# Performance work log

Measured on AMD Instinct MI355X. Metric: run time of the kernel, lower is better.

The kernel has to match this reference:

```python
import jax, jax.numpy as jnp
import numpy as np
import math

B, L, D, A, VD, H = 8, 2048, 1024, 1024, 1024, 1024
EPS = 1e-5

def gelu(x):
    return 0.5 * x * (1.0 + jax.lax.erf(x / math.sqrt(2.0)))

def setup_inputs() -> dict:
    key = jax.random.key(0)
    ks = jax.random.split(key, 12)
    s = 0.02
    return {
        "Q": jax.random.normal(ks[0], (B, L, D), jnp.float32),
        "K": jax.random.normal(ks[1], (B, L, D), jnp.float32),
        "V": jax.random.normal(ks[2], (B, L, D), jnp.float32),
        "attn_mask": jax.random.randint(ks[3], (B, L, L), 0, 2, jnp.int32),
        "Wq": jax.random.normal(ks[4], (D, A), jnp.float32) * s,
        "bq": jnp.zeros((A,), jnp.float32),
        "Wk": jax.random.normal(ks[5], (D, A), jnp.float32) * s,
        "bk": jnp.zeros((A,), jnp.float32),
        "Wv": jax.random.normal(ks[6], (D, VD), jnp.float32) * s,
        "bv": jnp.zeros((VD,), jnp.float32),
        "Wo": jax.random.normal(ks[7], (VD, H), jnp.float32) * s,
        "bo": jnp.zeros((H,), jnp.float32),
        "gamma": jnp.ones((H,), jnp.float32),
        "beta": jnp.zeros((H,), jnp.float32),
    }

def reference(Q, K, V, attn_mask, Wq, bq, Wk, bk, Wv, bv, Wo, bo, gamma, beta):
    q = Q @ Wq + bq                      # [B,L,A]
    k = K @ Wk + bk                      # [B,L,A]
    scores = jnp.einsum('bqa,bka->bqk', q, k) / math.sqrt(A)
    scores = scores + attn_mask.astype(jnp.float32) * (-1e9)
    scores = jnp.swapaxes(scores, -1, -2)  # [B,Lk,Lq]; softmax over QUERY axis
    attn = jax.nn.softmax(scores, axis=-1)
    wv = V @ Wv + bv                     # [B,L,VD]
    context = jnp.einsum('bkq,bqv->bkv', attn, wv)  # [B,L,VD]
    context = gelu(context @ Wo + bo)    # [B,L,H]
    mu = jnp.mean(context, axis=-1, keepdims=True)
    var = jnp.var(context, axis=-1, keepdims=True)
    context = (context - mu) / jnp.sqrt(var + EPS) * gamma + beta
    return context, attn
```

## Files before the change

### kernel.cpp

```cpp
#include <hip/hip_runtime.h>
#include <math.h>

typedef __bf16 bf16;
typedef __bf16 bf16x8 __attribute__((ext_vector_type(8)));
typedef __bf16 bf16x4 __attribute__((ext_vector_type(4)));
typedef float f32x4 __attribute__((ext_vector_type(4)));

__device__ inline void gload16(const void* g, void* l) {
  typedef __attribute__((address_space(1))) const unsigned int guint;
  typedef __attribute__((address_space(3))) unsigned int luint;
  __builtin_amdgcn_global_load_lds((guint*)g, (luint*)l, 16, 0, 0);
}

template<int BIAS_MODE, bool MASK, bool GELU, bool OUT_BF16>
__global__ __launch_bounds__(512, 2)
void bgemm8_k(const bf16* __restrict__ A, const bf16* __restrict__ B,
              const float* __restrict__ bias, const signed char* __restrict__ mT,
              void* __restrict__ Cout, int N, int ldc, int K,
              long sAb, long sBb, long sCb, long sMb, float scale)
{
  __shared__ bf16 As[4 * 8192];
  __shared__ bf16 Bs[4 * 8192];

  const int t    = threadIdx.x;
  const int zb   = blockIdx.z;
  const int gx   = gridDim.x;
  const int nwg  = gx * gridDim.y;
  const int orig = blockIdx.y * gx + blockIdx.x;
  const int swz  = (orig & 7) * (nwg >> 3) + (orig >> 3);
  const int m0   = (swz / gx) * 256;
  const int n0   = (swz % gx) * 256;

  const int wave = t >> 6;
  const int lane = t & 63;
  const int wm = wave >> 2;
  const int wn = wave & 3;
  const int fr = lane & 15;
  const int fg = lane >> 4;

  const bf16* Abase = A + (size_t)zb * sAb + (size_t)m0 * K;
  const bf16* Bbase = B + (size_t)zb * sBb + (size_t)n0 * K;
  size_t gOff[2];
  int    ldsOff[2];
#pragma unroll
  for (int j = 0; j < 2; ++j) {
    const int L   = j * 8192 + t * 16;
    const int row = L >> 6;
    const int gp  = (L >> 4) & 3;
    const int g   = gp ^ ((row >> 1) & 3);
    gOff[j]   = (size_t)row * K + (size_t)g * 8;
    ldsOff[j] = j * 4096 + wave * 512;
  }
  const int HMAX = (K >> 5) * 2;

  auto stage = [&](int H) {
    if (H >= HMAX) return;
    const int s    = H >> 1;
    const int slot = s & 3;
    const size_t kof = (size_t)s * 32;
    if ((H & 1) == 0) {
      gload16(Abase + kof + gOff[0], As + slot * 8192 + ldsOff[0]);
      gload16(Abase + kof + gOff[1], As + slot * 8192 + ldsOff[1]);
    } else {
      gload16(Bbase + kof + gOff[0], Bs + slot * 8192 + ldsOff[0]);
      gload16(Bbase + kof + gOff[1], Bs + slot * 8192 + ldsOff[1]);
    }
  };

  const int xsw  = (fg ^ ((fr >> 1) & 3)) * 8;
  const int aoff = (wm * 128 + fr) * 32 + xsw;
  const int boff = (wn * 64 + fr) * 32 + xsw;

  f32x4 acc[8][4] = {};
  const int T = K >> 6;

  stage(0); stage(1); stage(2); stage(3); stage(4);
  asm volatile("s_waitcnt vmcnt(6)" ::: "memory");
  __builtin_amdgcn_s_barrier();

  for (int tt = 0; tt < T; ++tt) {
#pragma unroll
    for (int p = 0; p < 4; ++p) {
      const int kk   = p & 1;
      const int oh   = p >> 1;
      const int slot = (2 * tt + kk) & 3;
      bf16x8 af[4], bfv[4];
#pragma unroll
      for (int i = 0; i < 4; ++i)
        af[i]  = *(const bf16x8*)(As + slot * 8192 + aoff + (oh * 4 + i) * 512);
#pragma unroll
      for (int i = 0; i < 4; ++i)
        bfv[i] = *(const bf16x8*)(Bs + slot * 8192 + boff + i * 512);
      stage(4 * tt + p + 5);
      __builtin_amdgcn_s_barrier();
      __builtin_amdgcn_s_setprio(1);
#pragma unroll
      for (int mi = 0; mi < 4; ++mi)
#pragma unroll
        for (int ni = 0; ni < 4; ++ni)
          acc[oh * 4 + mi][ni] =
            __builtin_amdgcn_mfma_f32_16x16x32_bf16(af[mi], bfv[ni], acc[oh * 4 + mi][ni], 0, 0, 0);
      __builtin_amdgcn_s_setprio(0);
      if (p == 0) {
        if (tt == T - 1) asm volatile("s_waitcnt vmcnt(0)" ::: "memory");
        else             asm volatile("s_waitcnt vmcnt(4)" ::: "memory");
      }
      if (p == 3) {
        if (tt < T - 2)       asm volatile("s_waitcnt vmcnt(6)" ::: "memory");
        else if (tt == T - 2) asm volatile("s_waitcnt vmcnt(4)" ::: "memory");
      }
      __builtin_amdgcn_s_barrier();
    }
  }

  const signed char* mb = mT + (size_t)zb * sMb;
#pragma unroll
  for (int mi = 0; mi < 8; ++mi) {
#pragma unroll
    for (int ni = 0; ni < 4; ++ni) {
      const int col = n0 + wn * 64 + ni * 16 + fr;
#pragma unroll
      for (int i = 0; i < 4; ++i) {
        const int r = m0 + wm * 128 + mi * 16 + fg * 4 + i;
        float v = acc[mi][ni][i] * scale;
        if constexpr (BIAS_MODE == 1) v += bias[col];
        if constexpr (BIAS_MODE == 2) v += bias[r];
        if constexpr (MASK) v += -1e9f * (float)mb[(size_t)r * N + col];
        if constexpr (GELU) v = 0.5f * v * (1.0f + erff(v * 0.70710678118f));
        const size_t off = (size_t)zb * sCb + (size_t)r * ldc + col;
        if constexpr (OUT_BF16) ((bf16*)Cout)[off] = (bf16)v;
        else                    ((float*)Cout)[off] = v;
      }
    }
  }
}

__global__ __launch_bounds__(256)
void conv_k(const float* __restrict__ in, bf16* __restrict__ out, long n8)
{
  for (long i = blockIdx.x * 256 + threadIdx.x; i < n8; i += (long)gridDim.x * 256) {
    f32x4 a = *(const f32x4*)(in + i * 8);
    f32x4 b = *(const f32x4*)(in + i * 8 + 4);
    bf16x8 o;
#pragma unroll
    for (int j = 0; j < 4; ++j) { o[j] = (bf16)a[j]; o[4 + j] = (bf16)b[j]; }
    *(bf16x8*)(out + i * 8) = o;
  }
}

__global__ __launch_bounds__(256)
void wtrans_k(const float* __restrict__ W0, const float* __restrict__ W1,
              const float* __restrict__ W2, const float* __restrict__ W3,
              bf16* __restrict__ out)
{
  const float* Ws[4] = {W0, W1, W2, W3};
  const float* W = Ws[blockIdx.z];
  bf16* o = out + (size_t)blockIdx.z * (1024 * 1024);
  __shared__ bf16 tile[64][72];
  const int t  = threadIdx.x;
  const int c0 = blockIdx.x * 64;
  const int r0 = blockIdx.y * 64;
  {
    const int rr = t >> 2;
    const int cc = (t & 3) * 16;
    const float* src = W + (size_t)(r0 + rr) * 1024 + c0 + cc;
#pragma unroll
    for (int j = 0; j < 16; j += 4) {
      f32x4 v = *(const f32x4*)(src + j);
#pragma unroll
      for (int i = 0; i < 4; ++i) tile[cc + j + i][rr] = (bf16)v[i];
    }
  }
  __syncthreads();
  {
    const int nr = t >> 2;
    const int kc = (t & 3) * 16;
    bf16* dst = o + (size_t)(c0 + nr) * 1024 + r0 + kc;
    *(bf16x8*)dst       = *(const bf16x8*)&tile[nr][kc];
    *(bf16x8*)(dst + 8) = *(const bf16x8*)&tile[nr][kc + 8];
  }
}

__global__ __launch_bounds__(256)
void maskT_k(const int* __restrict__ mask, signed char* __restrict__ mT)
{
  __shared__ signed char tile[64][65];
  const int t  = threadIdx.x;
  const int b  = blockIdx.z;
  const int k0 = blockIdx.x * 64;
  const int q0 = blockIdx.y * 64;
  {
    const int iq = t >> 2;
    const int ic = (t & 3) * 16;
    const int* src = mask + ((size_t)b * 2048 + q0 + iq) * 2048 + k0 + ic;
#pragma unroll
    for (int j = 0; j < 16; j += 4) {
      int4 v = *(const int4*)(src + j);
      tile[ic + j + 0][iq] = (signed char)v.x;
      tile[ic + j + 1][iq] = (signed char)v.y;
      tile[ic + j + 2][iq] = (signed char)v.z;
      tile[ic + j + 3][iq] = (signed char)v.w;
    }
  }
  __syncthreads();
  {
    const int ik = t >> 2;
    const int iq = (t & 3) * 16;
    signed char* dst = mT + ((size_t)b * 2048 + k0 + ik) * 2048 + q0 + iq;
#pragma unroll
    for (int j = 0; j < 16; ++j) dst[j] = tile[ik][iq + j];
  }
}

__global__ __launch_bounds__(256)
void softmax_rows_k(float* __restrict__ P, bf16* __restrict__ Pb)
{
  char* slot = (char*)P + (size_t)blockIdx.x * 8192;
  const bf16* pin = (const bf16*)slot;
  float* pout = (float*)slot;
  bf16* pb = Pb + (size_t)blockIdx.x * 2048;
  const int t = threadIdx.x;
  const int wave = t >> 6, lane = t & 63;
  bf16x8 raw = *(const bf16x8*)(pin + t * 8);
  float v[8];
#pragma unroll
  for (int j = 0; j < 8; ++j) v[j] = (float)raw[j];
  float m = -3e38f;
#pragma unroll
  for (int j = 0; j < 8; ++j) m = fmaxf(m, v[j]);
#pragma unroll
  for (int off = 32; off; off >>= 1) m = fmaxf(m, __shfl_xor(m, off));
  __shared__ float red[8];
  if (lane == 0) red[wave] = m;
  __syncthreads();
  m = fmaxf(fmaxf(red[0], red[1]), fmaxf(red[2], red[3]));
  float s = 0.0f;
#pragma unroll
  for (int j = 0; j < 8; ++j) { v[j] = __expf(v[j] - m); s += v[j]; }
#pragma unroll
  for (int off = 32; off; off >>= 1) s += __shfl_xor(s, off);
  if (lane == 0) red[4 + wave] = s;
  __syncthreads();
  s = red[4] + red[5] + red[6] + red[7];
  const float inv = 1.0f / s;
  f32x4 o0, o1;
  bf16x8 ob;
#pragma unroll
  for (int j = 0; j < 4; ++j) {
    o0[j] = v[j] * inv; o1[j] = v[4 + j] * inv;
    ob[j] = (bf16)o0[j]; ob[4 + j] = (bf16)o1[j];
  }
  __syncthreads();
  *(f32x4*)(pout + t * 8)     = o0;
  *(f32x4*)(pout + t * 8 + 4) = o1;
  *(bf16x8*)(pb + t * 8)      = ob;
}

__global__ __launch_bounds__(256)
void ln_k(const bf16* __restrict__ g, const float* __restrict__ gamma,
          const float* __restrict__ beta, float* __restrict__ out)
{
  const bf16* p = g + (size_t)blockIdx.x * 1024;
  const int t = threadIdx.x;
  const int wave = t >> 6, lane = t & 63;
  bf16x4 raw = *(const bf16x4*)(p + t * 4);
  f32x4 v;
#pragma unroll
  for (int j = 0; j < 4; ++j) v[j] = (float)raw[j];
  float s = v[0] + v[1] + v[2] + v[3];
  float q = v[0]*v[0] + v[1]*v[1] + v[2]*v[2] + v[3]*v[3];
#pragma unroll
  for (int off = 32; off; off >>= 1) { s += __shfl_xor(s, off); q += __shfl_xor(q, off); }
  __shared__ float red[16];
  if (lane == 0) { red[wave] = s; red[8 + wave] = q; }
  __syncthreads();
  s = red[0] + red[1] + red[2] + red[3];
  q = red[8] + red[9] + red[10] + red[11];
  const float mu   = s * (1.0f / 1024.0f);
  const float var  = q * (1.0f / 1024.0f) - mu * mu;
  const float rstd = rsqrtf(var + 1e-5f);
  f32x4 gm = *(const f32x4*)(gamma + t * 4);
  f32x4 bt = *(const f32x4*)(beta + t * 4);
  f32x4 o;
#pragma unroll
  for (int j = 0; j < 4; ++j) o[j] = (v[j] - mu) * rstd * gm[j] + bt[j];
  *(f32x4*)(out + (size_t)blockIdx.x * 1024 + t * 4) = o;
}

extern "C" void kernel_launch(void* const* d_in, const int* in_sizes, int n_in,
                              void* d_out, int out_size, void* d_ws, size_t ws_size,
                              hipStream_t stream)
{
  const float* Q     = (const float*)d_in[0];
  const float* Kin   = (const float*)d_in[1];
  const float* V     = (const float*)d_in[2];
  const int*   mask  = (const int*)d_in[3];
  const float* Wq    = (const float*)d_in[4];
  const float* bq    = (const float*)d_in[5];
  const float* Wk    = (const float*)d_in[6];
  const float* bk    = (const float*)d_in[7];
  const float* Wv    = (const float*)d_in[8];
  const float* bv    = (const float*)d_in[9];
  const float* Wo    = (const float*)d_in[10];
  const float* bo    = (const float*)d_in[11];
  const float* gamma = (const float*)d_in[12];
  const float* beta  = (const float*)d_in[13];

  float* outCtx  = (float*)d_out;
  float* outAttn = outCtx + (size_t)8 * 2048 * 1024;

  char* ws = (char*)d_ws;
  const size_t MB = 1048576;
  bf16*        wts   = (bf16*)(ws + 0 * MB);
  bf16*        qp    = (bf16*)(ws + 8 * MB);
  bf16*        kp    = (bf16*)(ws + 40 * MB);
  bf16*        Qb    = (bf16*)(ws + 72 * MB);
  bf16*        Kb    = (bf16*)(ws + 104 * MB);
  signed char* mT    = (signed char*)(ws + 72 * MB);
  bf16*        attnb = (bf16*)(ws + 40 * MB);
  bf16*        wvT   = (bf16*)(ws + 8 * MB);
  bf16*        Vb    = (bf16*)(ws + 104 * MB);
  bf16*        ctx   = (bf16*)(ws + 104 * MB);
  bf16*        g     = (bf16*)(ws + 40 * MB);
  bf16* Wqt = wts;
  bf16* Wkt = wts + 1 * 1024 * 1024;
  bf16* Wvt = wts + 2 * 1024 * 1024;
  bf16* Wot = wts + 3 * 1024 * 1024;

  const dim3 blk(256);
  const dim3 blk8(512);
  const long n8 = (long)16384 * 1024 / 8;

  wtrans_k<<<dim3(16, 16, 4), blk, 0, stream>>>(Wq, Wk, Wv, Wo, wts);
  conv_k<<<dim3(2048), blk, 0, stream>>>(Q, Qb, n8);
  conv_k<<<dim3(2048), blk, 0, stream>>>(Kin, Kb, n8);
  bgemm8_k<1, false, false, true><<<dim3(4, 64, 1), blk8, 0, stream>>>(
      Qb, Wqt, bq, nullptr, qp, 1024, 1024, 1024, 0, 0, 0, 0, 1.0f);
  bgemm8_k<1, false, false, true><<<dim3(4, 64, 1), blk8, 0, stream>>>(
      Kb, Wkt, bk, nullptr, kp, 1024, 1024, 1024, 0, 0, 0, 0, 1.0f);
  conv_k<<<dim3(2048), blk, 0, stream>>>(V, Vb, n8);
  maskT_k<<<dim3(32, 32, 8), blk, 0, stream>>>(mask, mT);
  bgemm8_k<0, true, false, true><<<dim3(8, 8, 8), blk8, 0, stream>>>(
      kp, qp, nullptr, mT, (bf16*)outAttn, 2048, 4096, 1024,
      (long)2048 * 1024, (long)2048 * 1024, (long)2048 * 4096, (long)2048 * 2048, 0.03125f);
  bgemm8_k<2, false, false, true><<<dim3(8, 4, 8), blk8, 0, stream>>>(
      Wvt, Vb, bv, nullptr, wvT, 2048, 2048, 1024,
      0, (long)2048 * 1024, (long)1024 * 2048, 0, 1.0f);
  softmax_rows_k<<<dim3(16384), blk, 0, stream>>>(outAttn, attnb);
  bgemm8_k<0, false, false, true><<<dim3(4, 8, 8), blk8, 0, stream>>>(
      attnb, wvT, nullptr, nullptr, ctx, 1024, 1024, 2048,
      (long)2048 * 2048, (long)1024 * 2048, (long)2048 * 1024, 0, 1.0f);
  bgemm8_k<1, false, true, true><<<dim3(4, 64, 1), blk8, 0, stream>>>(
      ctx, Wot, bo, nullptr, g, 1024, 1024, 1024, 0, 0, 0, 0, 1.0f);
  ln_k<<<dim3(16384), blk, 0, stream>>>(g, gamma, beta, outCtx);
}
```

Before: 505.9 us.

## Stage GEMM epilogue through LDS for vectorized stores; batch Q/K projections

The bf16 GEMM epilogue now writes results into a swizzled per-wave LDS buffer, then reads them back as 8-element vectors, applies the mask with 8-byte int8 loads and issues 16-byte global stores. The old path did scalar 2-byte stores and byte mask loads. The Q and K conversions are merged into one two-slice launch, and the Q and K projections into one batched GEMM that picks its bias per slice. A redundant __syncthreads in softmax is dropped, and the epilogue adds a block-wide barrier and LDS round trip.

Result: faster. 489.6 us (-3.2%).

```diff
diff --git a/kernel.cpp b/kernel.cpp
--- a/kernel.cpp
+++ b/kernel.cpp
@@ -5,6 +5,7 @@
 typedef __bf16 bf16x8 __attribute__((ext_vector_type(8)));
 typedef __bf16 bf16x4 __attribute__((ext_vector_type(4)));
 typedef float f32x4 __attribute__((ext_vector_type(4)));
+typedef signed char schar8 __attribute__((ext_vector_type(8)));
 
 __device__ inline void gload16(const void* g, void* l) {
   typedef __attribute__((address_space(1))) const unsigned int guint;
@@ -15,12 +16,14 @@
 template<int BIAS_MODE, bool MASK, bool GELU, bool OUT_BF16>
 __global__ __launch_bounds__(512, 2)
 void bgemm8_k(const bf16* __restrict__ A, const bf16* __restrict__ B,
-              const float* __restrict__ bias, const signed char* __restrict__ mT,
+              const float* __restrict__ bias, const float* __restrict__ bias2,
+              const signed char* __restrict__ mT,
               void* __restrict__ Cout, int N, int ldc, int K,
               long sAb, long sBb, long sCb, long sMb, float scale)
 {
-  __shared__ bf16 As[4 * 8192];
-  __shared__ bf16 Bs[4 * 8192];
+  __shared__ __align__(16) char smem[131072];
+  bf16* As = (bf16*)smem;
+  bf16* Bs = (bf16*)(smem + 65536);
 
   const int t    = threadIdx.x;
   const int zb   = blockIdx.z;
@@ -30,6 +33,8 @@
   const int swz  = (orig & 7) * (nwg >> 3) + (orig >> 3);
   const int m0   = (swz / gx) * 256;
   const int n0   = (swz % gx) * 256;
+
+  const float* bp = (BIAS_MODE && bias2 && zb) ? bias2 : bias;
 
   const int wave = t >> 6;
   const int lane = t & 63;
@@ -113,31 +118,70 @@
     }
   }
 
-  const signed char* mb = mT + (size_t)zb * sMb;
-#pragma unroll
-  for (int mi = 0; mi < 8; ++mi) {
-#pragma unroll
-    for (int ni = 0; ni < 4; ++ni) {
-      const int col = n0 + wn * 64 + ni * 16 + fr;
-#pragma unroll
-      for (int i = 0; i < 4; ++i) {
-        const int r = m0 + wm * 128 + mi * 16 + fg * 4 + i;
-        float v = acc[mi][ni][i] * scale;
-        if constexpr (BIAS_MODE == 1) v += bias[col];
-        if constexpr (BIAS_MODE == 2) v += bias[r];
-        if constexpr (MASK) v += -1e9f * (float)mb[(size_t)r * N + col];
-        if constexpr (GELU) v = 0.5f * v * (1.0f + erff(v * 0.70710678118f));
-        const size_t off = (size_t)zb * sCb + (size_t)r * ldc + col;
-        if constexpr (OUT_BF16) ((bf16*)Cout)[off] = (bf16)v;
-        else                    ((float*)Cout)[off] = v;
-      }
-    }
-  }
-}
-
-__global__ __launch_bounds__(256)
-void conv_k(const float* __restrict__ in, bf16* __restrict__ out, long n8)
-{
+  if constexpr (OUT_BF16) {
+    bf16* wbuf = (bf16*)(smem + wave * 16384);
+#pragma unroll
+    for (int mi = 0; mi < 8; ++mi) {
+#pragma unroll
+      for (int ni = 0; ni < 4; ++ni) {
+        const int col = n0 + wn * 64 + ni * 16 + fr;
+#pragma unroll
+        for (int i = 0; i < 4; ++i) {
+          const int r = mi * 16 + fg * 4 + i;
+          float v = acc[mi][ni][i] * scale;
+          if constexpr (BIAS_MODE == 1) v += bp[col];
+          if constexpr (BIAS_MODE == 2) v += bp[m0 + wm * 128 + r];
+          if constexpr (GELU) v = 0.5f * v * (1.0f + erff(v * 0.70710678118f));
+          const int cb = ni * 32 + fr * 2;
+          *(bf16*)((char*)wbuf + r * 128 + (cb ^ ((r & 7) << 4))) = (bf16)v;
+        }
+      }
+    }
+    __syncthreads();
+    const int rowbase = m0 + wm * 128;
+    const int colbase = n0 + wn * 64;
+    const signed char* mb = MASK ? (mT + (size_t)zb * sMb) : nullptr;
+#pragma unroll
+    for (int j = 0; j < 16; ++j) {
+      const int r  = j * 8 + (lane >> 3);
+      const int cg = lane & 7;
+      bf16x8 val = *(const bf16x8*)((char*)wbuf + r * 128 + ((cg << 4) ^ ((r & 7) << 4)));
+      const int grow = rowbase + r;
+      const int gcol = colbase + cg * 8;
+      if constexpr (MASK) {
+        schar8 mk = *(const schar8*)(mb + (size_t)grow * N + gcol);
+#pragma unroll
+        for (int e = 0; e < 8; ++e)
+          val[e] = (bf16)((float)val[e] + -1e9f * (float)mk[e]);
+      }
+      *(bf16x8*)((bf16*)Cout + (size_t)zb * sCb + (size_t)grow * ldc + gcol) = val;
+    }
+  } else {
+#pragma unroll
+    for (int mi = 0; mi < 8; ++mi) {
+#pragma unroll
+      for (int ni = 0; ni < 4; ++ni) {
+        const int col = n0 + wn * 64 + ni * 16 + fr;
+#pragma unroll
+        for (int i = 0; i < 4; ++i) {
+          const int r = m0 + wm * 128 + mi * 16 + fg * 4 + i;
+          float v = acc[mi][ni][i] * scale;
+          if constexpr (BIAS_MODE == 1) v += bp[col];
+          if constexpr (BIAS_MODE == 2) v += bp[r];
+          if constexpr (GELU) v = 0.5f * v * (1.0f + erff(v * 0.70710678118f));
+          ((float*)Cout)[(size_t)zb * sCb + (size_t)r * ldc + col] = v;
+        }
+      }
+    }
+  }
+}
+
+__global__ __launch_bounds__(256)
+void conv2_k(const float* __restrict__ i0, const float* __restrict__ i1,
+             bf16* __restrict__ o0, bf16* __restrict__ o1, long n8)
+{
+  const float* in = blockIdx.z ? i1 : i0;
+  bf16* out = blockIdx.z ? o1 : o0;
   for (long i = blockIdx.x * 256 + threadIdx.x; i < n8; i += (long)gridDim.x * 256) {
     f32x4 a = *(const f32x4*)(in + i * 8);
     f32x4 b = *(const f32x4*)(in + i * 8 + 4);
@@ -250,7 +294,6 @@
     o0[j] = v[j] * inv; o1[j] = v[4 + j] * inv;
     ob[j] = (bf16)o0[j]; ob[4 + j] = (bf16)o1[j];
   }
-  __syncthreads();
   *(f32x4*)(pout + t * 8)     = o0;
   *(f32x4*)(pout + t * 8 + 4) = o1;
   *(bf16x8*)(pb + t * 8)      = ob;
@@ -332,25 +375,23 @@
   const long n8 = (long)16384 * 1024 / 8;
 
   wtrans_k<<<dim3(16, 16, 4), blk, 0, stream>>>(Wq, Wk, Wv, Wo, wts);
-  conv_k<<<dim3(2048), blk, 0, stream>>>(Q, Qb, n8);
-  conv_k<<<dim3(2048), blk, 0, stream>>>(Kin, Kb, n8);
-  bgemm8_k<1, false, false, true><<<dim3(4, 64, 1), blk8, 0, stream>>>(
-      Qb, Wqt, bq, nullptr, qp, 1024, 1024, 1024, 0, 0, 0, 0, 1.0f);
-  bgemm8_k<1, false, false, true><<<dim3(4, 64, 1), blk8, 0, stream>>>(
-      Kb, Wkt, bk, nullptr, kp, 1024, 1024, 1024, 0, 0, 0, 0, 1.0f);
-  conv_k<<<dim3(2048), blk, 0, stream>>>(V, Vb, n8);
+  conv2_k<<<dim3(2048, 1, 2), blk, 0, stream>>>(Q, Kin, Qb, Kb, n8);
+  bgemm8_k<1, false, false, true><<<dim3(4, 64, 2), blk8, 0, stream>>>(
+      Qb, Wqt, bq, bk, nullptr, qp, 1024, 1024, 1024,
+      16777216, 1048576, 16777216, 0, 1.0f);
+  conv2_k<<<dim3(2048, 1, 1), blk, 0, stream>>>(V, nullptr, Vb, nullptr, n8);
   maskT_k<<<dim3(32, 32, 8), blk, 0, stream>>>(mask, mT);
   bgemm8_k<0, true, false, true><<<dim3(8, 8, 8), blk8, 0, stream>>>(
-      kp, qp, nullptr, mT, (bf16*)outAttn, 2048, 4096, 1024,
+      kp, qp, nullptr, nullptr, mT, (bf16*)outAttn, 2048, 4096, 1024,
       (long)2048 * 1024, (long)2048 * 1024, (long)2048 * 4096, (long)2048 * 2048, 0.03125f);
   bgemm8_k<2, false, false, true><<<dim3(8, 4, 8), blk8, 0, stream>>>(
-      Wvt, Vb, bv, nullptr, wvT, 2048, 2048, 1024,
+      Wvt, Vb, bv, nullptr, nullptr, wvT, 2048, 2048, 1024,
       0, (long)2048 * 1024, (long)1024 * 2048, 0, 1.0f);
   softmax_rows_k<<<dim3(16384), blk, 0, stream>>>(outAttn, attnb);
   bgemm8_k<0, false, false, true><<<dim3(4, 8, 8), blk8, 0, stream>>>(
-      attnb, wvT, nullptr, nullptr, ctx, 1024, 1024, 2048,
+      attnb, wvT, nullptr, nullptr, nullptr, ctx, 1024, 1024, 2048,
       (long)2048 * 2048, (long)1024 * 2048, (long)2048 * 1024, 0, 1.0f);
   bgemm8_k<1, false, true, true><<<dim3(4, 64, 1), blk8, 0, stream>>>(
-      ctx, Wot, bo, nullptr, g, 1024, 1024, 1024, 0, 0, 0, 0, 1.0f);
+      ctx, Wot, bo, nullptr, nullptr, g, 1024, 1024, 1024, 0, 0, 0, 0, 1.0f);
   ln_k<<<dim3(16384), blk, 0, stream>>>(g, gamma, beta, outCtx);
 }
```
